# Kernel optimization log

Measured on AMD Instinct MI355X. Metric: run time of the kernel, lower is better.

## Reference

```python
import jax, jax.numpy as jnp
import numpy as np

H = 8
SPLIT = 1
# deterministic stand-in for random.shuffle(range(8)) in the original
_PERM = np.random.RandomState(0).permutation(H)
SERIES_IDX = jnp.asarray(_PERM[SPLIT:])  # 7 heads
CROSS_IDX = jnp.asarray(_PERM[:SPLIT])   # 1 head


def setup_inputs() -> dict:
    key = jax.random.key(0)
    ks = jax.random.split(key, 5)
    B, L, E = 8, 1024, 64
    shp = (B, L, H, E)
    return {
        "queries": jax.random.normal(ks[0], shp, dtype=jnp.float32),
        "keys": jax.random.normal(ks[1], shp, dtype=jnp.float32),
        "keysT": jax.random.normal(ks[2], shp, dtype=jnp.float32),
        "values": jax.random.normal(ks[3], shp, dtype=jnp.float32),
        "valuesT": jax.random.normal(ks[4], shp, dtype=jnp.float32),
    }


def reference(queries, keys, keysT, values, valuesT):
    B, L, _, E = queries.shape
    scale = 1.0 / jnp.sqrt(jnp.asarray(E, dtype=queries.dtype))
    neg_inf = jnp.asarray(-jnp.inf, dtype=queries.dtype)

    # head split (gather along head dim)
    sq = queries[:, :, SERIES_IDX]   # [B,L,7,E]
    sk = keys[:, :, SERIES_IDX]      # [B,S,7,E]
    sv = values[:, :, SERIES_IDX]    # [B,S,7,D]
    cq = queries[:, :, CROSS_IDX]    # [B,L,1,E]
    ckT = keysT[:, :, CROSS_IDX]     # [B,C,1,E]
    cvT = valuesT[:, :, CROSS_IDX]   # [B,C,1,D]

    # causal mask: True above the diagonal -> disallowed
    causal = jnp.triu(jnp.ones((L, L), dtype=bool), k=1)  # [L,L]

    # series branch
    scores = jnp.einsum('blne,bsne->bnls', sq, sk)  # [B,7,L,S]
    scores = jnp.where(causal[None, None], neg_inf, scores * scale)
    series = jax.nn.softmax(scores, axis=-1)
    V = jnp.einsum('bhls,bshd->blhd', series, sv)   # [B,L,7,D]

    # cross branch
    cscores = jnp.einsum('blme,bcme->bmlc', cq, ckT)  # [B,1,L,C]
    cscores = jnp.where(causal[None, None], neg_inf, cscores * scale)
    crosses = jax.nn.softmax(cscores, axis=-1)
    V_cross = jnp.einsum('bhlc,bchd->blhd', crosses, cvT)  # [B,L,1,D]

    return jnp.concatenate([V, V_cross], axis=2)  # [B,L,8,D]
```

## Files before the change

kernel.cpp:

```cpp
#include <hip/hip_runtime.h>
#include <math.h>

#define Lq 1024
#define Hq 8
#define Eq 64
#define LDW 72
#define PTW 40
#define KV_SH (64 * LDW)
#define BUF_SH (2 * KV_SH)

#define SRC_HEAD_PACKED 0x64503712u

#if __has_builtin(__builtin_amdgcn_mfma_f32_16x16x16bf16_1k)
#define HAVE_MFMA16 1
#else
#define HAVE_MFMA16 0
#endif

typedef __bf16 bf16_t;
typedef __bf16 bf16x8 __attribute__((ext_vector_type(8)));
typedef __bf16 bf16x4 __attribute__((ext_vector_type(4)));
typedef short short4v __attribute__((ext_vector_type(4)));
typedef float floatx4 __attribute__((ext_vector_type(4)));

__device__ __forceinline__ bf16x8 cvt8(const float4 a, const float4 b) {
    bf16x8 r;
    r[0] = (bf16_t)a.x; r[1] = (bf16_t)a.y; r[2] = (bf16_t)a.z; r[3] = (bf16_t)a.w;
    r[4] = (bf16_t)b.x; r[5] = (bf16_t)b.y; r[6] = (bf16_t)b.z; r[7] = (bf16_t)b.w;
    return r;
}

__device__ __forceinline__ void block_sync_lds() {
    asm volatile("s_waitcnt lgkmcnt(0)" ::: "memory");
    __builtin_amdgcn_s_barrier();
    __builtin_amdgcn_sched_barrier(0);
}

__global__ __launch_bounds__(512, 4)
void attn_mfma(const float* __restrict__ Q, const float* __restrict__ Ks,
               const float* __restrict__ KTs, const float* __restrict__ Vs,
               const float* __restrict__ VTs, float* __restrict__ out) {
    const int slot = blockIdx.x;
    const int b    = blockIdx.y;
    const int qt   = 15 - blockIdx.z;
    const int h    = (SRC_HEAD_PACKED >> (slot * 4)) & 0xF;
    const float* __restrict__ Kp = (slot == 7) ? KTs : Ks;
    const float* __restrict__ Vp = (slot == 7) ? VTs : Vs;

    const int tid  = threadIdx.x;
    const int wv   = tid >> 6;
    const int lane = tid & 63;
    const int ln16 = lane & 15;
    const int quad = lane >> 4;
    const int wq   = wv & 3;
    const int kh   = wv >> 2;

    __shared__ alignas(16) unsigned short smem[2 * BUF_SH + (1 - HAVE_MFMA16) * 8 * 16 * PTW];
#if !HAVE_MFMA16
    unsigned short (*pt)[PTW] = (unsigned short (*)[PTW])(smem + 2 * BUF_SH + wv * 16 * PTW);
#endif

    const float qs = 0.125f * 1.44269504f;
    bf16x8 qf[2];
    {
        const int r = qt * 64 + wq * 16 + ln16;
        const float* qa = Q + (((size_t)b * Lq + r) * Hq + h) * Eq + quad * 8;
        #pragma unroll
        for (int ec = 0; ec < 2; ++ec) {
            float4 f0 = ((const float4*)(qa + ec * 32))[0];
            float4 f1 = ((const float4*)(qa + ec * 32))[1];
            f0.x*=qs; f0.y*=qs; f0.z*=qs; f0.w*=qs;
            f1.x*=qs; f1.y*=qs; f1.z*=qs; f1.w*=qs;
            qf[ec] = cvt8(f0, f1);
        }
    }

    floatx4 O[4];
    #pragma unroll
    for (int i = 0; i < 4; ++i) O[i] = (floatx4){0, 0, 0, 0};
    float m = -1e30f, l = 0.f;

    float4 kq[2];
    float  vq[8];
    const int kj = tid >> 3, kc = (tid & 7) * 8;
    const int vd = tid & 63, vk = wv * 8;

    auto load_tile = [&](int kt) {
        const float* kb = Kp + (((size_t)b * Lq + kt * 64 + kj) * Hq + h) * Eq + kc;
        kq[0] = ((const float4*)kb)[0]; kq[1] = ((const float4*)kb)[1];
        const float* vb = Vp + (((size_t)b * Lq + kt * 64 + vk) * Hq + h) * Eq + vd;
        #pragma unroll
        for (int i = 0; i < 8; ++i) vq[i] = vb[(size_t)i * (Hq * Eq)];
    };
    auto stage = [&](int bsel) {
        unsigned short* dst = smem + bsel * BUF_SH;
        *(bf16x8*)&dst[kj * LDW + kc] = cvt8(kq[0], kq[1]);
        const float4* vq4 = (const float4*)vq;
        *(bf16x8*)&dst[KV_SH + vd * LDW + vk] = cvt8(vq4[0], vq4[1]);
    };

    load_tile(0);
    stage(0);
    load_tile(1);
    block_sync_lds();

    for (int kt = 0; kt <= qt; ++kt) {
        const unsigned short* base = smem + (kt & 1) * BUF_SH;

        bf16x8 kf[2][2];
        #pragma unroll
        for (int c = 0; c < 2; ++c) {
            kf[c][0] = *(const bf16x8*)&base[((kh * 2 + c) * 16 + ln16) * LDW + quad * 8];
            kf[c][1] = *(const bf16x8*)&base[((kh * 2 + c) * 16 + ln16) * LDW + 32 + quad * 8];
        }
        if (kt < qt) stage((kt + 1) & 1);
        if (kt + 1 < qt) load_tile(kt + 2);

        floatx4 s[2];
        #pragma unroll
        for (int nc = 0; nc < 2; ++nc) {
            floatx4 acc = (floatx4){0, 0, 0, 0};
            acc = __builtin_amdgcn_mfma_f32_16x16x32_bf16(kf[nc][0], qf[0], acc, 0, 0, 0);
            acc = __builtin_amdgcn_mfma_f32_16x16x32_bf16(kf[nc][1], qf[1], acc, 0, 0, 0);
            s[nc] = acc;
        }

#if HAVE_MFMA16
        bf16x4 va[4][2];
        #pragma unroll
        for (int dc = 0; dc < 4; ++dc)
            #pragma unroll
            for (int nc = 0; nc < 2; ++nc)
                va[dc][nc] = *(const bf16x4*)&base[KV_SH + (dc * 16 + ln16) * LDW + kh * 32 + nc * 16 + quad * 4];
#else
        bf16x8 vf[4];
        #pragma unroll
        for (int c = 0; c < 4; ++c)
            vf[c] = *(const bf16x8*)&base[KV_SH + (c * 16 + ln16) * LDW + kh * 32 + quad * 8];
#endif

        if (kt == qt) {
            const int rin = wq * 16 + ln16;
            #pragma unroll
            for (int nc = 0; nc < 2; ++nc)
                #pragma unroll
                for (int r = 0; r < 4; ++r)
                    if (kh * 32 + nc * 16 + quad * 4 + r > rin) s[nc][r] = -INFINITY;
        }
        float mn = s[0][0];
        #pragma unroll
        for (int nc = 0; nc < 2; ++nc)
            #pragma unroll
            for (int r = 0; r < 4; ++r) mn = fmaxf(mn, s[nc][r]);
        mn = fmaxf(mn, __shfl_xor(mn, 16, 64));
        mn = fmaxf(mn, __shfl_xor(mn, 32, 64));
        mn = fmaxf(mn, m);
        const float alpha = __builtin_amdgcn_exp2f(m - mn);
        m = mn;
        float ps = 0.f;
        float pv[2][4];
        #pragma unroll
        for (int nc = 0; nc < 2; ++nc)
            #pragma unroll
            for (int r = 0; r < 4; ++r) {
                pv[nc][r] = __builtin_amdgcn_exp2f(s[nc][r] - mn);
                ps += pv[nc][r];
            }
        ps += __shfl_xor(ps, 16, 64);
        ps += __shfl_xor(ps, 32, 64);
        l = l * alpha + ps;
        #pragma unroll
        for (int dc = 0; dc < 4; ++dc) O[dc] *= alpha;

#if HAVE_MFMA16
        short4v pb[2];
        #pragma unroll
        for (int nc = 0; nc < 2; ++nc) {
            bf16x4 t;
            t[0] = (bf16_t)pv[nc][0]; t[1] = (bf16_t)pv[nc][1];
            t[2] = (bf16_t)pv[nc][2]; t[3] = (bf16_t)pv[nc][3];
            pb[nc] = __builtin_bit_cast(short4v, t);
        }
        #pragma unroll
        for (int dc = 0; dc < 4; ++dc)
            #pragma unroll
            for (int nc = 0; nc < 2; ++nc)
                O[dc] = __builtin_amdgcn_mfma_f32_16x16x16bf16_1k(
                    __builtin_bit_cast(short4v, va[dc][nc]), pb[nc], O[dc], 0, 0, 0);
#else
        #pragma unroll
        for (int nc = 0; nc < 2; ++nc) {
            bf16x4 pk;
            pk[0] = (bf16_t)pv[nc][0]; pk[1] = (bf16_t)pv[nc][1];
            pk[2] = (bf16_t)pv[nc][2]; pk[3] = (bf16_t)pv[nc][3];
            *(bf16x4*)&pt[ln16][nc * 16 + quad * 4] = pk;
        }
        bf16x8 pf = *(const bf16x8*)&pt[ln16][quad * 8];
        #pragma unroll
        for (int dc = 0; dc < 4; ++dc)
            O[dc] = __builtin_amdgcn_mfma_f32_16x16x32_bf16(vf[dc], pf, O[dc], 0, 0, 0);
#endif

        block_sync_lds();
    }

    float* mb = (float*)smem;
    if (kh) {
        float* dst = mb + (wq * 64 + lane) * 18;
        #pragma unroll
        for (int dc = 0; dc < 4; ++dc) {
            *(float2*)(dst + dc * 4)     = make_float2(O[dc][0], O[dc][1]);
            *(float2*)(dst + dc * 4 + 2) = make_float2(O[dc][2], O[dc][3]);
        }
        dst[16] = m; dst[17] = l;
    }
    __syncthreads();
    if (!kh) {
        const float* src = mb + (wq * 64 + lane) * 18;
        const float m1 = src[16], l1 = src[17];
        const float mm = fmaxf(m, m1);
        const float a0 = __builtin_amdgcn_exp2f(m - mm);
        const float a1 = __builtin_amdgcn_exp2f(m1 - mm);
        const float inv = 1.0f / (l * a0 + l1 * a1);
        const int row = qt * 64 + wq * 16 + ln16;
        float* op = out + (((size_t)b * Lq + row) * Hq + slot) * Eq + quad * 4;
        #pragma unroll
        for (int dc = 0; dc < 4; ++dc) {
            float4 o;
            o.x = (O[dc][0] * a0 + src[dc * 4 + 0] * a1) * inv;
            o.y = (O[dc][1] * a0 + src[dc * 4 + 1] * a1) * inv;
            o.z = (O[dc][2] * a0 + src[dc * 4 + 2] * a1) * inv;
            o.w = (O[dc][3] * a0 + src[dc * 4 + 3] * a1) * inv;
            *(float4*)(op + dc * 16) = o;
        }
    }
}

extern "C" void kernel_launch(void* const* d_in, const int* in_sizes, int n_in,
                              void* d_out, int out_size, void* d_ws, size_t ws_size,
                              hipStream_t stream) {
    const float* queries = (const float*)d_in[0];
    const float* keys    = (const float*)d_in[1];
    const float* keysT   = (const float*)d_in[2];
    const float* values  = (const float*)d_in[3];
    const float* valuesT = (const float*)d_in[4];
    float* out = (float*)d_out;

    dim3 grid(Hq, 8, 16);
    dim3 block(512);
    attn_mfma<<<grid, block, 0, stream>>>(queries, keys, keysT, values, valuesT, out);
}
```

Before: 134.0 us.

## Pair causal query tiles per block and share K/V tiles across them

Each block now handles two query tiles, p and 15-p, so causal work is balanced across blocks and every staged K/V tile serves both tiles. The block shrinks to 256 threads, and each wave keeps four 16-row query groups in registers, which raises per-wave MFMA reuse of the K/V fragments. The aim is to cut redundant global loads and conversions of K/V and to even out the triangular workload. In exchange, register pressure rises (16 accumulator vectors per wave), the grid halves, and waves for the shorter tile sit idle during the later iterations.

```diff
diff --git a/kernel.cpp b/kernel.cpp
--- a/kernel.cpp
+++ b/kernel.cpp
@@ -5,17 +5,10 @@
 #define Hq 8
 #define Eq 64
 #define LDW 72
-#define PTW 40
 #define KV_SH (64 * LDW)
 #define BUF_SH (2 * KV_SH)
 
 #define SRC_HEAD_PACKED 0x64503712u
-
-#if __has_builtin(__builtin_amdgcn_mfma_f32_16x16x16bf16_1k)
-#define HAVE_MFMA16 1
-#else
-#define HAVE_MFMA16 0
-#endif
 
 typedef __bf16 bf16_t;
 typedef __bf16 bf16x8 __attribute__((ext_vector_type(8)));
@@ -36,34 +29,34 @@
     __builtin_amdgcn_sched_barrier(0);
 }
 
-__global__ __launch_bounds__(512, 4)
+__global__ __launch_bounds__(256, 2)
 void attn_mfma(const float* __restrict__ Q, const float* __restrict__ Ks,
                const float* __restrict__ KTs, const float* __restrict__ Vs,
                const float* __restrict__ VTs, float* __restrict__ out) {
     const int slot = blockIdx.x;
     const int b    = blockIdx.y;
-    const int qt   = 15 - blockIdx.z;
+    const int p    = blockIdx.z;
     const int h    = (SRC_HEAD_PACKED >> (slot * 4)) & 0xF;
     const float* __restrict__ Kp = (slot == 7) ? KTs : Ks;
     const float* __restrict__ Vp = (slot == 7) ? VTs : Vs;
+    const int pA = p, pB = 15 - p;
 
     const int tid  = threadIdx.x;
     const int wv   = tid >> 6;
     const int lane = tid & 63;
     const int ln16 = lane & 15;
     const int quad = lane >> 4;
-    const int wq   = wv & 3;
-    const int kh   = wv >> 2;
-
-    __shared__ alignas(16) unsigned short smem[2 * BUF_SH + (1 - HAVE_MFMA16) * 8 * 16 * PTW];
-#if !HAVE_MFMA16
-    unsigned short (*pt)[PTW] = (unsigned short (*)[PTW])(smem + 2 * BUF_SH + wv * 16 * PTW);
-#endif
+    const int tb   = wv >> 1;
+    const int kh   = wv & 1;
+    const int pT   = tb ? pB : pA;
+
+    __shared__ alignas(16) unsigned short smem[2 * BUF_SH];
 
     const float qs = 0.125f * 1.44269504f;
-    bf16x8 qf[2];
-    {
-        const int r = qt * 64 + wq * 16 + ln16;
+    bf16x8 qf[4][2];
+    #pragma unroll
+    for (int qg = 0; qg < 4; ++qg) {
+        const int r = pT * 64 + qg * 16 + ln16;
         const float* qa = Q + (((size_t)b * Lq + r) * Hq + h) * Eq + quad * 8;
         #pragma unroll
         for (int ec = 0; ec < 2; ++ec) {
@@ -71,32 +64,38 @@
             float4 f1 = ((const float4*)(qa + ec * 32))[1];
             f0.x*=qs; f0.y*=qs; f0.z*=qs; f0.w*=qs;
             f1.x*=qs; f1.y*=qs; f1.z*=qs; f1.w*=qs;
-            qf[ec] = cvt8(f0, f1);
-        }
-    }
-
-    floatx4 O[4];
+            qf[qg][ec] = cvt8(f0, f1);
+        }
+    }
+
+    floatx4 O[4][4];
     #pragma unroll
-    for (int i = 0; i < 4; ++i) O[i] = (floatx4){0, 0, 0, 0};
-    float m = -1e30f, l = 0.f;
-
-    float4 kq[2];
-    float  vq[8];
-    const int kj = tid >> 3, kc = (tid & 7) * 8;
-    const int vd = tid & 63, vk = wv * 8;
+    for (int qg = 0; qg < 4; ++qg)
+        #pragma unroll
+        for (int dc = 0; dc < 4; ++dc) O[qg][dc] = (floatx4){0, 0, 0, 0};
+    float mq[4] = {-1e30f, -1e30f, -1e30f, -1e30f};
+    float lq[4] = {0.f, 0.f, 0.f, 0.f};
+
+    float4 kq[4];
+    float  vq[16];
+    const int kj = tid >> 2, kc = (tid & 3) * 16;
+    const int vd = lane,     vk = wv * 16;
 
     auto load_tile = [&](int kt) {
         const float* kb = Kp + (((size_t)b * Lq + kt * 64 + kj) * Hq + h) * Eq + kc;
         kq[0] = ((const float4*)kb)[0]; kq[1] = ((const float4*)kb)[1];
+        kq[2] = ((const float4*)kb)[2]; kq[3] = ((const float4*)kb)[3];
         const float* vb = Vp + (((size_t)b * Lq + kt * 64 + vk) * Hq + h) * Eq + vd;
         #pragma unroll
-        for (int i = 0; i < 8; ++i) vq[i] = vb[(size_t)i * (Hq * Eq)];
+        for (int i = 0; i < 16; ++i) vq[i] = vb[(size_t)i * (Hq * Eq)];
     };
     auto stage = [&](int bsel) {
         unsigned short* dst = smem + bsel * BUF_SH;
-        *(bf16x8*)&dst[kj * LDW + kc] = cvt8(kq[0], kq[1]);
+        *(bf16x8*)&dst[kj * LDW + kc]     = cvt8(kq[0], kq[1]);
+        *(bf16x8*)&dst[kj * LDW + kc + 8] = cvt8(kq[2], kq[3]);
         const float4* vq4 = (const float4*)vq;
-        *(bf16x8*)&dst[KV_SH + vd * LDW + vk] = cvt8(vq4[0], vq4[1]);
+        *(bf16x8*)&dst[KV_SH + vd * LDW + vk]     = cvt8(vq4[0], vq4[1]);
+        *(bf16x8*)&dst[KV_SH + vd * LDW + vk + 8] = cvt8(vq4[2], vq4[3]);
     };
 
     load_tile(0);
@@ -104,134 +103,128 @@
     load_tile(1);
     block_sync_lds();
 
-    for (int kt = 0; kt <= qt; ++kt) {
+    for (int kt = 0; kt <= pB; ++kt) {
         const unsigned short* base = smem + (kt & 1) * BUF_SH;
+        const bool act = (kt <= pT);
 
         bf16x8 kf[2][2];
-        #pragma unroll
-        for (int c = 0; c < 2; ++c) {
-            kf[c][0] = *(const bf16x8*)&base[((kh * 2 + c) * 16 + ln16) * LDW + quad * 8];
-            kf[c][1] = *(const bf16x8*)&base[((kh * 2 + c) * 16 + ln16) * LDW + 32 + quad * 8];
-        }
-        if (kt < qt) stage((kt + 1) & 1);
-        if (kt + 1 < qt) load_tile(kt + 2);
-
-        floatx4 s[2];
-        #pragma unroll
-        for (int nc = 0; nc < 2; ++nc) {
-            floatx4 acc = (floatx4){0, 0, 0, 0};
-            acc = __builtin_amdgcn_mfma_f32_16x16x32_bf16(kf[nc][0], qf[0], acc, 0, 0, 0);
-            acc = __builtin_amdgcn_mfma_f32_16x16x32_bf16(kf[nc][1], qf[1], acc, 0, 0, 0);
-            s[nc] = acc;
-        }
-
-#if HAVE_MFMA16
-        bf16x4 va[4][2];
-        #pragma unroll
-        for (int dc = 0; dc < 4; ++dc)
-            #pragma unroll
-            for (int nc = 0; nc < 2; ++nc)
-                va[dc][nc] = *(const bf16x4*)&base[KV_SH + (dc * 16 + ln16) * LDW + kh * 32 + nc * 16 + quad * 4];
-#else
-        bf16x8 vf[4];
-        #pragma unroll
-        for (int c = 0; c < 4; ++c)
-            vf[c] = *(const bf16x8*)&base[KV_SH + (c * 16 + ln16) * LDW + kh * 32 + quad * 8];
-#endif
-
-        if (kt == qt) {
-            const int rin = wq * 16 + ln16;
-            #pragma unroll
-            for (int nc = 0; nc < 2; ++nc)
-                #pragma unroll
-                for (int r = 0; r < 4; ++r)
-                    if (kh * 32 + nc * 16 + quad * 4 + r > rin) s[nc][r] = -INFINITY;
-        }
-        float mn = s[0][0];
-        #pragma unroll
-        for (int nc = 0; nc < 2; ++nc)
-            #pragma unroll
-            for (int r = 0; r < 4; ++r) mn = fmaxf(mn, s[nc][r]);
-        mn = fmaxf(mn, __shfl_xor(mn, 16, 64));
-        mn = fmaxf(mn, __shfl_xor(mn, 32, 64));
-        mn = fmaxf(mn, m);
-        const float alpha = __builtin_amdgcn_exp2f(m - mn);
-        m = mn;
-        float ps = 0.f;
-        float pv[2][4];
-        #pragma unroll
-        for (int nc = 0; nc < 2; ++nc)
-            #pragma unroll
-            for (int r = 0; r < 4; ++r) {
-                pv[nc][r] = __builtin_amdgcn_exp2f(s[nc][r] - mn);
-                ps += pv[nc][r];
-            }
-        ps += __shfl_xor(ps, 16, 64);
-        ps += __shfl_xor(ps, 32, 64);
-        l = l * alpha + ps;
-        #pragma unroll
-        for (int dc = 0; dc < 4; ++dc) O[dc] *= alpha;
-
-#if HAVE_MFMA16
-        short4v pb[2];
-        #pragma unroll
-        for (int nc = 0; nc < 2; ++nc) {
-            bf16x4 t;
-            t[0] = (bf16_t)pv[nc][0]; t[1] = (bf16_t)pv[nc][1];
-            t[2] = (bf16_t)pv[nc][2]; t[3] = (bf16_t)pv[nc][3];
-            pb[nc] = __builtin_bit_cast(short4v, t);
-        }
-        #pragma unroll
-        for (int dc = 0; dc < 4; ++dc)
-            #pragma unroll
-            for (int nc = 0; nc < 2; ++nc)
-                O[dc] = __builtin_amdgcn_mfma_f32_16x16x16bf16_1k(
-                    __builtin_bit_cast(short4v, va[dc][nc]), pb[nc], O[dc], 0, 0, 0);
-#else
-        #pragma unroll
-        for (int nc = 0; nc < 2; ++nc) {
-            bf16x4 pk;
-            pk[0] = (bf16_t)pv[nc][0]; pk[1] = (bf16_t)pv[nc][1];
-            pk[2] = (bf16_t)pv[nc][2]; pk[3] = (bf16_t)pv[nc][3];
-            *(bf16x4*)&pt[ln16][nc * 16 + quad * 4] = pk;
-        }
-        bf16x8 pf = *(const bf16x8*)&pt[ln16][quad * 8];
-        #pragma unroll
-        for (int dc = 0; dc < 4; ++dc)
-            O[dc] = __builtin_amdgcn_mfma_f32_16x16x32_bf16(vf[dc], pf, O[dc], 0, 0, 0);
-#endif
-
+        if (act) {
+            #pragma unroll
+            for (int c = 0; c < 2; ++c) {
+                kf[c][0] = *(const bf16x8*)&base[((kh * 2 + c) * 16 + ln16) * LDW + quad * 8];
+                kf[c][1] = *(const bf16x8*)&base[((kh * 2 + c) * 16 + ln16) * LDW + 32 + quad * 8];
+            }
+        }
+        if (kt < pB) stage((kt + 1) & 1);
+        if (kt + 1 < pB) load_tile(kt + 2);
+
+        if (act) {
+            bf16x4 va[4][2];
+            #pragma unroll
+            for (int dc = 0; dc < 4; ++dc)
+                #pragma unroll
+                for (int nc = 0; nc < 2; ++nc)
+                    va[dc][nc] = *(const bf16x4*)&base[KV_SH + (dc * 16 + ln16) * LDW + kh * 32 + nc * 16 + quad * 4];
+
+            const bool diag = (kt == pT);
+            #pragma unroll
+            for (int qg = 0; qg < 4; ++qg) {
+                if (diag && kh && qg < 2) continue;
+
+                floatx4 s[2];
+                #pragma unroll
+                for (int nc = 0; nc < 2; ++nc) {
+                    floatx4 acc = (floatx4){0, 0, 0, 0};
+                    acc = __builtin_amdgcn_mfma_f32_16x16x32_bf16(kf[nc][0], qf[qg][0], acc, 0, 0, 0);
+                    acc = __builtin_amdgcn_mfma_f32_16x16x32_bf16(kf[nc][1], qf[qg][1], acc, 0, 0, 0);
+                    s[nc] = acc;
+                }
+                if (diag) {
+                    const int rin = qg * 16 + ln16;
+                    #pragma unroll
+                    for (int nc = 0; nc < 2; ++nc)
+                        #pragma unroll
+                        for (int r = 0; r < 4; ++r)
+                            if (kh * 32 + nc * 16 + quad * 4 + r > rin) s[nc][r] = -INFINITY;
+                }
+                float mn = s[0][0];
+                #pragma unroll
+                for (int nc = 0; nc < 2; ++nc)
+                    #pragma unroll
+                    for (int r = 0; r < 4; ++r) mn = fmaxf(mn, s[nc][r]);
+                mn = fmaxf(mn, __shfl_xor(mn, 16, 64));
+                mn = fmaxf(mn, __shfl_xor(mn, 32, 64));
+                mn = fmaxf(mn, mq[qg]);
+                const float alpha = __builtin_amdgcn_exp2f(mq[qg] - mn);
+                mq[qg] = mn;
+                float ps = 0.f;
+                float pv[2][4];
+                #pragma unroll
+                for (int nc = 0; nc < 2; ++nc)
+                    #pragma unroll
+                    for (int r = 0; r < 4; ++r) {
+                        pv[nc][r] = __builtin_amdgcn_exp2f(s[nc][r] - mn);
+                        ps += pv[nc][r];
+                    }
+                ps += __shfl_xor(ps, 16, 64);
+                ps += __shfl_xor(ps, 32, 64);
+                lq[qg] = lq[qg] * alpha + ps;
+                #pragma unroll
+                for (int dc = 0; dc < 4; ++dc) O[qg][dc] *= alpha;
+
+                short4v pb[2];
+                #pragma unroll
+                for (int nc = 0; nc < 2; ++nc) {
+                    bf16x4 t;
+                    t[0] = (bf16_t)pv[nc][0]; t[1] = (bf16_t)pv[nc][1];
+                    t[2] = (bf16_t)pv[nc][2]; t[3] = (bf16_t)pv[nc][3];
+                    pb[nc] = __builtin_bit_cast(short4v, t);
+                }
+                #pragma unroll
+                for (int dc = 0; dc < 4; ++dc)
+                    #pragma unroll
+                    for (int nc = 0; nc < 2; ++nc)
+                        O[qg][dc] = __builtin_amdgcn_mfma_f32_16x16x16bf16_1k(
+                            __builtin_bit_cast(short4v, va[dc][nc]), pb[nc], O[qg][dc], 0, 0, 0);
+            }
+        }
         block_sync_lds();
     }
 
-    float* mb = (float*)smem;
+    float* mb = (float*)smem + tb * 4608;
     if (kh) {
-        float* dst = mb + (wq * 64 + lane) * 18;
-        #pragma unroll
-        for (int dc = 0; dc < 4; ++dc) {
-            *(float2*)(dst + dc * 4)     = make_float2(O[dc][0], O[dc][1]);
-            *(float2*)(dst + dc * 4 + 2) = make_float2(O[dc][2], O[dc][3]);
-        }
-        dst[16] = m; dst[17] = l;
+        #pragma unroll
+        for (int qg = 0; qg < 4; ++qg) {
+            float* dst = mb + (qg * 64 + lane) * 18;
+            #pragma unroll
+            for (int dc = 0; dc < 4; ++dc) {
+                *(float2*)(dst + dc * 4)     = make_float2(O[qg][dc][0], O[qg][dc][1]);
+                *(float2*)(dst + dc * 4 + 2) = make_float2(O[qg][dc][2], O[qg][dc][3]);
+            }
+            dst[16] = mq[qg]; dst[17] = lq[qg];
+        }
     }
     __syncthreads();
     if (!kh) {
-        const float* src = mb + (wq * 64 + lane) * 18;
-        const float m1 = src[16], l1 = src[17];
-        const float mm = fmaxf(m, m1);
-        const float a0 = __builtin_amdgcn_exp2f(m - mm);
-        const float a1 = __builtin_amdgcn_exp2f(m1 - mm);
-        const float inv = 1.0f / (l * a0 + l1 * a1);
-        const int row = qt * 64 + wq * 16 + ln16;
-        float* op = out + (((size_t)b * Lq + row) * Hq + slot) * Eq + quad * 4;
-        #pragma unroll
-        for (int dc = 0; dc < 4; ++dc) {
-            float4 o;
-            o.x = (O[dc][0] * a0 + src[dc * 4 + 0] * a1) * inv;
-            o.y = (O[dc][1] * a0 + src[dc * 4 + 1] * a1) * inv;
-            o.z = (O[dc][2] * a0 + src[dc * 4 + 2] * a1) * inv;
-            o.w = (O[dc][3] * a0 + src[dc * 4 + 3] * a1) * inv;
-            *(float4*)(op + dc * 16) = o;
+        #pragma unroll
+        for (int qg = 0; qg < 4; ++qg) {
+            const float* src = mb + (qg * 64 + lane) * 18;
+            const float m1 = src[16], l1 = src[17];
+            const float mm = fmaxf(mq[qg], m1);
+            const float a0 = __builtin_amdgcn_exp2f(mq[qg] - mm);
+            const float a1 = __builtin_amdgcn_exp2f(m1 - mm);
+            const float inv = 1.0f / (lq[qg] * a0 + l1 * a1);
+            const int row = pT * 64 + qg * 16 + ln16;
+            float* op = out + (((size_t)b * Lq + row) * Hq + slot) * Eq + quad * 4;
+            #pragma unroll
+            for (int dc = 0; dc < 4; ++dc) {
+                float4 o;
+                o.x = (O[qg][dc][0] * a0 + src[dc * 4 + 0] * a1) * inv;
+                o.y = (O[qg][dc][1] * a0 + src[dc * 4 + 1] * a1) * inv;
+                o.z = (O[qg][dc][2] * a0 + src[dc * 4 + 2] * a1) * inv;
+                o.w = (O[qg][dc][3] * a0 + src[dc * 4 + 3] * a1) * inv;
+                *(float4*)(op + dc * 16) = o;
+            }
         }
     }
 }
@@ -246,7 +239,7 @@
     const float* valuesT = (const float*)d_in[4];
     float* out = (float*)d_out;
 
-    dim3 grid(Hq, 8, 16);
-    dim3 block(512);
+    dim3 grid(Hq, 8, 8);
+    dim3 block(256);
     attn_mfma<<<grid, block, 0, stream>>>(queries, keys, keysT, values, valuesT, out);
 }
```

Result: slower. 143.1 us (+6.8%).
